# Optimization experiments

Hardware: AMD Instinct MI355X
Metric: run time of the kernel (lower is better)

Reference implementation:

```python
import jax, jax.numpy as jnp
import numpy as np

HIDDEN = 512


def setup_inputs() -> dict:
    key = jax.random.key(0)
    k1, k2, k3, k4, k5 = jax.random.split(key, 5)
    scale = 1.0 / np.sqrt(HIDDEN)
    return {
        "decoder_hidden": jax.random.normal(k1, (64, HIDDEN), dtype=jnp.float32),
        "encoder_outputs": jax.random.normal(k2, (4096, 64, HIDDEN), dtype=jnp.float32),
        "W1": jax.random.uniform(k3, (HIDDEN, HIDDEN), jnp.float32, -scale, scale),
        "W2": jax.random.uniform(k4, (HIDDEN, HIDDEN), jnp.float32, -scale, scale),
        "v": jax.random.uniform(k5, (HIDDEN,), jnp.float32, -scale, scale),
    }


def reference(decoder_hidden, encoder_outputs, W1, W2, v):
    # decoder_hidden: (B, H); encoder_outputs: (S, B, H)
    enc = jnp.transpose(encoder_outputs, (1, 0, 2))          # (B, S, H)
    dec_proj = decoder_hidden @ W1.T                          # (B, H) — no need to repeat over S
    enc_proj = jnp.einsum('bsh,gh->bsg', enc, W2)             # (B, S, H)
    energy = jnp.tanh(dec_proj[:, None, :] + enc_proj) @ v    # (B, S)
    attn_weights = jax.nn.softmax(energy, axis=1)             # (B, S)
    context = jnp.einsum('bs,bsh->bh', attn_weights, enc)     # (B, H)
    return (context, attn_weights)
```

## Files before the change

kernel.cpp:

```cpp
#include <hip/hip_runtime.h>
#include <math.h>


#define BATCH 64
#define SEQ   4096
#define HID   512

typedef __attribute__((ext_vector_type(8))) short bf16x8;
typedef __attribute__((ext_vector_type(4))) float f32x4;

__device__ __forceinline__ float fast_tanh(float x) {
    return 1.0f - 2.0f / (__expf(2.0f * x) + 1.0f);
}

__device__ __forceinline__ unsigned cvt2(float lo, float hi) {
    unsigned r;
    asm("v_cvt_pk_bf16_f32 %0, %1, %2" : "=v"(r) : "v"(lo), "v"(hi));
    return r;
}

__device__ __forceinline__ void gload_lds16(const void* g, void* l) {
    __builtin_amdgcn_global_load_lds(
        (const __attribute__((address_space(1))) unsigned*)g,
        (__attribute__((address_space(3))) unsigned*)l, 16, 0, 0);
}

__global__ void k_cvtW2(const float* __restrict__ W2, ushort* __restrict__ W2t)
{
    const int n  = blockIdx.x * 256 + threadIdx.x;
    const int kb = n >> 11;
    const int f  = n & 2047;
    const int g  = f >> 2, rg = f & 3;
    const float* src = W2 + (size_t)g * HID + kb * 32 + rg * 8;
    const float4 x = *reinterpret_cast<const float4*>(src);
    const float4 y = *reinterpret_cast<const float4*>(src + 4);
    uint4 u;
    u.x = cvt2(x.x, x.y);  u.y = cvt2(x.z, x.w);
    u.z = cvt2(y.x, y.y);  u.w = cvt2(y.z, y.w);
    const int slot = f ^ ((f >> 3) & 7);
    *reinterpret_cast<uint4*>(W2t + (size_t)kb * 16384 + slot * 8) = u;
}

__global__ void k_decproj(const float* __restrict__ dh,
                          const float* __restrict__ W1,
                          float* __restrict__ dp)
{
    __shared__ float wrow[HID];
    const int g = blockIdx.x;
    const int t = threadIdx.x;
    for (int i = t; i < HID; i += 256) wrow[i] = W1[g * HID + i];
    __syncthreads();

    const int b = t >> 2, q = t & 3;
    const float* dhb = dh + b * HID + q * 128;
    const float* wr  = wrow + q * 128;
    float acc = 0.f;
    #pragma unroll 8
    for (int i = 0; i < 128; i += 4) {
        const float4 d4 = *reinterpret_cast<const float4*>(dhb + i);
        acc = fmaf(d4.x, wr[i + 0], acc);
        acc = fmaf(d4.y, wr[i + 1], acc);
        acc = fmaf(d4.z, wr[i + 2], acc);
        acc = fmaf(d4.w, wr[i + 3], acc);
    }
    acc += __shfl_xor(acc, 1);
    acc += __shfl_xor(acc, 2);
    if (q == 0) dp[b * HID + g] = acc;
}

#define LDA 40

__global__ __launch_bounds__(256, 4)
void k_energy(const float* __restrict__ enc, const ushort* __restrict__ W2t,
              const float* __restrict__ dp,  const float* __restrict__ v,
              float* __restrict__ eparts)
{
    __shared__ __align__(16) ushort As[64 * LDA];
    __shared__ __align__(16) ushort Bs[2][8192];
    __shared__ float part[4][64];

    const int idx  = blockIdx.x;
    const int g16  = idx >> 4, rr = idx & 15;
    const int gh   = rr >> 3;
    const int pair = (g16 << 3) | (rr & 7);
    const int schunk = pair & 63;
    const int b      = pair >> 6;
    const int s0     = schunk * 64;

    const int t    = threadIdx.x;
    const int lane = t & 63;
    const int wv   = t >> 6;
    const int gl   = lane & 15, rg = lane >> 4;

    f32x4 acc[4][4];
    const f32x4 z = {0.f, 0.f, 0.f, 0.f};
    #pragma unroll
    for (int m = 0; m < 4; ++m)
        #pragma unroll
        for (int n = 0; n < 4; ++n) acc[m][n] = z;

    const int arow = t >> 2, akq = t & 3;
    const float* aptr = enc + ((size_t)(s0 + arow) * BATCH + b) * HID + akq * 8;

    const ushort* Ap  = As + gl * LDA + rg * 8;
    const int bbase   = ((wv * 256 + gl * 4 + rg) ^ ((gl >> 1) & 7)) * 8;
    const ushort* Bp0 = &Bs[0][bbase];
    const ushort* Bp1 = &Bs[1][bbase];

    const char* wsrc = (const char*)W2t + gh * 16384;

    #pragma unroll
    for (int q = 0; q < 4; ++q)
        gload_lds16(wsrc + (q * 256 + t) * 16,
                    (char*)&Bs[0][0] + (q * 256 + t) * 16);
    float4 a0 = *reinterpret_cast<const float4*>(aptr);
    float4 a1 = *reinterpret_cast<const float4*>(aptr + 4);

    #pragma unroll
    for (int kb = 0; kb < 16; ++kb) {
        __syncthreads();
        {
            uint4 aw;
            aw.x = cvt2(a0.x, a0.y);  aw.y = cvt2(a0.z, a0.w);
            aw.z = cvt2(a1.x, a1.y);  aw.w = cvt2(a1.z, a1.w);
            *reinterpret_cast<uint4*>(&As[arow * LDA + akq * 8]) = aw;
        }
        __syncthreads();

        if (kb < 15) {
            const char* src = wsrc + (size_t)(kb + 1) * 32768;
            #pragma unroll
            for (int q = 0; q < 4; ++q)
                gload_lds16(src + (q * 256 + t) * 16,
                            (char*)&Bs[(kb + 1) & 1][0] + (q * 256 + t) * 16);
            a0 = *reinterpret_cast<const float4*>(aptr + (kb + 1) * 32);
            a1 = *reinterpret_cast<const float4*>(aptr + (kb + 1) * 32 + 4);
        }

        const ushort* Bp = (kb & 1) ? Bp1 : Bp0;
        bf16x8 af[4], bfr[4];
        #pragma unroll
        for (int m = 0; m < 4; ++m)
            af[m] = *reinterpret_cast<const bf16x8*>(Ap + m * 640);
        #pragma unroll
        for (int n = 0; n < 4; ++n)
            bfr[n] = *reinterpret_cast<const bf16x8*>(Bp + n * 512);
        #pragma unroll
        for (int m = 0; m < 4; ++m)
            #pragma unroll
            for (int n = 0; n < 4; ++n)
                acc[m][n] = __builtin_amdgcn_mfma_f32_16x16x32_bf16(
                    af[m], bfr[n], acc[m][n], 0, 0, 0);
    }

    float dpv[4], vv[4];
    #pragma unroll
    for (int n = 0; n < 4; ++n) {
        const int g = gh * 256 + wv * 64 + n * 16 + gl;
        dpv[n] = dp[b * HID + g];
        vv[n]  = v[g];
    }
    float p[4][4];
    #pragma unroll
    for (int m = 0; m < 4; ++m)
        #pragma unroll
        for (int r = 0; r < 4; ++r) p[m][r] = 0.f;
    #pragma unroll
    for (int n = 0; n < 4; ++n)
        #pragma unroll
        for (int m = 0; m < 4; ++m)
            #pragma unroll
            for (int r = 0; r < 4; ++r)
                p[m][r] += fast_tanh(dpv[n] + acc[m][n][r]) * vv[n];

    #pragma unroll
    for (int m = 0; m < 4; ++m)
        #pragma unroll
        for (int r = 0; r < 4; ++r) {
            float x = p[m][r];
            x += __shfl_xor(x, 1);
            x += __shfl_xor(x, 2);
            x += __shfl_xor(x, 4);
            x += __shfl_xor(x, 8);
            p[m][r] = x;
        }
    if (gl == 0) {
        #pragma unroll
        for (int m = 0; m < 4; ++m)
            #pragma unroll
            for (int r = 0; r < 4; ++r)
                part[wv][m * 16 + rg * 4 + r] = p[m][r];
    }
    __syncthreads();

    if (t < 64) {
        const float e = part[0][t] + part[1][t] + part[2][t] + part[3][t];
        eparts[(size_t)gh * BATCH * SEQ + (size_t)b * SEQ + s0 + t] = e;
    }
}

__global__ void k_softmax(const float* __restrict__ eparts,
                          float* __restrict__ attn)
{
    __shared__ float redm[4], reds[4];
    const int b = blockIdx.x, t = threadIdx.x;
    const float* e0 = eparts + (size_t)b * SEQ;
    const float* e1 = eparts + (size_t)BATCH * SEQ + (size_t)b * SEQ;

    float4 ev[4];
    float m = -3.4e38f;
    #pragma unroll
    for (int i = 0; i < 4; ++i) {
        const float4 x = *reinterpret_cast<const float4*>(e0 + i * 1024 + t * 4);
        const float4 y = *reinterpret_cast<const float4*>(e1 + i * 1024 + t * 4);
        ev[i] = make_float4(x.x + y.x, x.y + y.y, x.z + y.z, x.w + y.w);
        m = fmaxf(m, fmaxf(fmaxf(ev[i].x, ev[i].y), fmaxf(ev[i].z, ev[i].w)));
    }
    #pragma unroll
    for (int off = 1; off < 64; off <<= 1) m = fmaxf(m, __shfl_xor(m, off));
    if ((t & 63) == 0) redm[t >> 6] = m;
    __syncthreads();
    m = fmaxf(fmaxf(redm[0], redm[1]), fmaxf(redm[2], redm[3]));

    float s = 0.f;
    #pragma unroll
    for (int i = 0; i < 4; ++i) {
        ev[i].x = __expf(ev[i].x - m);  ev[i].y = __expf(ev[i].y - m);
        ev[i].z = __expf(ev[i].z - m);  ev[i].w = __expf(ev[i].w - m);
        s += (ev[i].x + ev[i].y) + (ev[i].z + ev[i].w);
    }
    #pragma unroll
    for (int off = 1; off < 64; off <<= 1) s += __shfl_xor(s, off);
    if ((t & 63) == 0) reds[t >> 6] = s;
    __syncthreads();
    s = (reds[0] + reds[1]) + (reds[2] + reds[3]);
    const float inv = 1.0f / s;

    float* o = attn + (size_t)b * SEQ;
    #pragma unroll
    for (int i = 0; i < 4; ++i) {
        const float4 w4 = make_float4(ev[i].x * inv, ev[i].y * inv,
                                      ev[i].z * inv, ev[i].w * inv);
        *reinterpret_cast<float4*>(o + i * 1024 + t * 4) = w4;
    }
}

__global__ void k_ctxpart(const float* __restrict__ enc,
                          const float* __restrict__ attn,
                          float* __restrict__ pctx)
{
    __shared__ float w[256];
    const int b  = blockIdx.x;
    const int sp = blockIdx.y;
    const int t  = threadIdx.x;

    w[t] = attn[(size_t)b * SEQ + sp * 256 + t];
    __syncthreads();

    const float2* e2 = reinterpret_cast<const float2*>(enc);
    size_t idx = ((size_t)sp * 256 * BATCH + b) * (HID / 2) + t;
    const size_t stride = (size_t)BATCH * (HID / 2);

    float ax = 0.f, ay = 0.f;
    #pragma unroll 4
    for (int s = 0; s < 256; ++s) {
        const float2 ev = e2[idx];
        const float ws = w[s];
        ax = fmaf(ws, ev.x, ax);
        ay = fmaf(ws, ev.y, ay);
        idx += stride;
    }
    float2* p2 = reinterpret_cast<float2*>(pctx);
    p2[((size_t)sp * BATCH + b) * (HID / 2) + t] = make_float2(ax, ay);
}

__global__ void k_ctxsum(const float* __restrict__ pctx,
                         float* __restrict__ ctx)
{
    const int i = blockIdx.x * 256 + threadIdx.x;
    float s = 0.f;
    #pragma unroll
    for (int sp = 0; sp < 16; ++sp) s += pctx[(size_t)sp * BATCH * HID + i];
    ctx[i] = s;
}

extern "C" void kernel_launch(void* const* d_in, const int* in_sizes, int n_in,
                              void* d_out, int out_size, void* d_ws, size_t ws_size,
                              hipStream_t stream)
{
    const float* dh  = (const float*)d_in[0];
    const float* enc = (const float*)d_in[1];
    const float* W1  = (const float*)d_in[2];
    const float* W2  = (const float*)d_in[3];
    const float* v   = (const float*)d_in[4];

    float* out  = (float*)d_out;
    float* ctx  = out;
    float* attn = out + BATCH * HID;

    float*  dp      = (float*)d_ws;
    ushort* W2t     = (ushort*)(dp + BATCH * HID);
    float*  shared2 = (float*)(W2t + HID * HID);
    float*  eparts  = shared2;
    float*  pctx    = shared2;

    k_cvtW2  <<<128, 256, 0, stream>>>(W2, W2t);
    k_decproj<<<HID, 256, 0, stream>>>(dh, W1, dp);
    k_energy <<<8192, 256, 0, stream>>>(enc, W2t, dp, v, eparts);
    k_softmax<<<BATCH, 256, 0, stream>>>(eparts, attn);
    k_ctxpart<<<dim3(BATCH, 16), 256, 0, stream>>>(enc, attn, pctx);
    k_ctxsum <<<BATCH * HID / 256, 256, 0, stream>>>(pctx, ctx);
}
```

Before: 341.7 us.

## Load W2 fragments directly from global and double-buffer A tile in LDS

Pre-arranges the bf16 W2 copy into a per-wave, per-fragment layout so each lane can read its MFMA B operand straight from global or L2, removing the LDS staging of W2. The A tile (encoder rows) becomes double-buffered in LDS with a two-stage register prefetch, cutting the loop from two barriers per k-step to one. The cost is per-lane global latency on B loads inside the MFMA loop, relying on cache hits since all blocks share W2. LDS use also drops, which may allow more blocks per CU.

```diff
diff --git a/kernel.cpp b/kernel.cpp
--- a/kernel.cpp
+++ b/kernel.cpp
@@ -19,26 +19,23 @@
     return r;
 }
 
-__device__ __forceinline__ void gload_lds16(const void* g, void* l) {
-    __builtin_amdgcn_global_load_lds(
-        (const __attribute__((address_space(1))) unsigned*)g,
-        (__attribute__((address_space(3))) unsigned*)l, 16, 0, 0);
-}
-
 __global__ void k_cvtW2(const float* __restrict__ W2, ushort* __restrict__ W2t)
 {
     const int n  = blockIdx.x * 256 + threadIdx.x;
-    const int kb = n >> 11;
-    const int f  = n & 2047;
-    const int g  = f >> 2, rg = f & 3;
-    const float* src = W2 + (size_t)g * HID + kb * 32 + rg * 8;
+    const int g  = n >> 6, kc = n & 63;
+    const int kb = kc >> 2, rgl = kc & 3;
+    const int gh = g >> 8, wv = (g >> 6) & 3, fn = (g >> 4) & 3, gl = g & 15;
+
+    const float* src = W2 + (size_t)g * HID + kc * 8;
     const float4 x = *reinterpret_cast<const float4*>(src);
     const float4 y = *reinterpret_cast<const float4*>(src + 4);
     uint4 u;
     u.x = cvt2(x.x, x.y);  u.y = cvt2(x.z, x.w);
     u.z = cvt2(y.x, y.y);  u.w = cvt2(y.z, y.w);
-    const int slot = f ^ ((f >> 3) & 7);
-    *reinterpret_cast<uint4*>(W2t + (size_t)kb * 16384 + slot * 8) = u;
+
+    const size_t dst = (size_t)gh * 131072 + kb * 8192 + wv * 2048 + fn * 512
+                     + (rgl * 16 + gl) * 8;
+    *reinterpret_cast<uint4*>(W2t + dst) = u;
 }
 
 __global__ void k_decproj(const float* __restrict__ dh,
@@ -75,8 +72,7 @@
               const float* __restrict__ dp,  const float* __restrict__ v,
               float* __restrict__ eparts)
 {
-    __shared__ __align__(16) ushort As[64 * LDA];
-    __shared__ __align__(16) ushort Bs[2][8192];
+    __shared__ __align__(16) ushort As[2][64 * LDA];
     __shared__ float part[4][64];
 
     const int idx  = blockIdx.x;
@@ -101,56 +97,58 @@
 
     const int arow = t >> 2, akq = t & 3;
     const float* aptr = enc + ((size_t)(s0 + arow) * BATCH + b) * HID + akq * 8;
-
-    const ushort* Ap  = As + gl * LDA + rg * 8;
-    const int bbase   = ((wv * 256 + gl * 4 + rg) ^ ((gl >> 1) & 7)) * 8;
-    const ushort* Bp0 = &Bs[0][bbase];
-    const ushort* Bp1 = &Bs[1][bbase];
-
-    const char* wsrc = (const char*)W2t + gh * 16384;
-
-    #pragma unroll
-    for (int q = 0; q < 4; ++q)
-        gload_lds16(wsrc + (q * 256 + t) * 16,
-                    (char*)&Bs[0][0] + (q * 256 + t) * 16);
+    ushort* Aw0 = &As[0][arow * LDA + akq * 8];
+    ushort* Aw1 = &As[1][arow * LDA + akq * 8];
+
+    const ushort* Ap0 = &As[0][gl * LDA + rg * 8];
+    const ushort* Ap1 = &As[1][gl * LDA + rg * 8];
+
+    const ushort* bptr = W2t + (size_t)gh * 131072 + wv * 2048 + lane * 8;
+
     float4 a0 = *reinterpret_cast<const float4*>(aptr);
     float4 a1 = *reinterpret_cast<const float4*>(aptr + 4);
+    {
+        uint4 aw;
+        aw.x = cvt2(a0.x, a0.y);  aw.y = cvt2(a0.z, a0.w);
+        aw.z = cvt2(a1.x, a1.y);  aw.w = cvt2(a1.z, a1.w);
+        *reinterpret_cast<uint4*>(Aw0) = aw;
+    }
+    a0 = *reinterpret_cast<const float4*>(aptr + 32);
+    a1 = *reinterpret_cast<const float4*>(aptr + 36);
+    __syncthreads();
 
     #pragma unroll
     for (int kb = 0; kb < 16; ++kb) {
-        __syncthreads();
-        {
+        bf16x8 bfr[4];
+        #pragma unroll
+        for (int n = 0; n < 4; ++n)
+            bfr[n] = *reinterpret_cast<const bf16x8*>(bptr + kb * 8192 + n * 512);
+
+        const ushort* Ap = (kb & 1) ? Ap1 : Ap0;
+        bf16x8 af[4];
+        #pragma unroll
+        for (int m = 0; m < 4; ++m)
+            af[m] = *reinterpret_cast<const bf16x8*>(Ap + m * 16 * LDA);
+
+        if (kb < 15) {
             uint4 aw;
             aw.x = cvt2(a0.x, a0.y);  aw.y = cvt2(a0.z, a0.w);
             aw.z = cvt2(a1.x, a1.y);  aw.w = cvt2(a1.z, a1.w);
-            *reinterpret_cast<uint4*>(&As[arow * LDA + akq * 8]) = aw;
+            *reinterpret_cast<uint4*>((kb & 1) ? Aw0 : Aw1) = aw;
         }
-        __syncthreads();
-
-        if (kb < 15) {
-            const char* src = wsrc + (size_t)(kb + 1) * 32768;
-            #pragma unroll
-            for (int q = 0; q < 4; ++q)
-                gload_lds16(src + (q * 256 + t) * 16,
-                            (char*)&Bs[(kb + 1) & 1][0] + (q * 256 + t) * 16);
-            a0 = *reinterpret_cast<const float4*>(aptr + (kb + 1) * 32);
-            a1 = *reinterpret_cast<const float4*>(aptr + (kb + 1) * 32 + 4);
+        if (kb < 14) {
+            a0 = *reinterpret_cast<const float4*>(aptr + (kb + 2) * 32);
+            a1 = *reinterpret_cast<const float4*>(aptr + (kb + 2) * 32 + 4);
         }
 
-        const ushort* Bp = (kb & 1) ? Bp1 : Bp0;
-        bf16x8 af[4], bfr[4];
-        #pragma unroll
-        for (int m = 0; m < 4; ++m)
-            af[m] = *reinterpret_cast<const bf16x8*>(Ap + m * 640);
-        #pragma unroll
-        for (int n = 0; n < 4; ++n)
-            bfr[n] = *reinterpret_cast<const bf16x8*>(Bp + n * 512);
         #pragma unroll
         for (int m = 0; m < 4; ++m)
             #pragma unroll
             for (int n = 0; n < 4; ++n)
                 acc[m][n] = __builtin_amdgcn_mfma_f32_16x16x32_bf16(
                     af[m], bfr[n], acc[m][n], 0, 0, 0);
+
+        __syncthreads();
     }
 
     float dpv[4], vv[4];
```

Result: faster. 328.0 us (-4.0%).
